# Performance work log

Hardware: AMD Instinct MI355X
Metric: run time of the kernel (lower is better)

Reference implementation:

```python
import jax, jax.numpy as jnp
import numpy as np

B, T, D, H, L, K = 64, 512, 256, 256, 2, 3


def setup_inputs() -> dict:
    key = jax.random.key(0)
    ks = jax.random.split(key, 12)
    s = 0.05
    f = jnp.float32
    return {
        "x": jax.random.normal(ks[0], (B, T, D), f),
        # GRUCell params per layer (torch gate order: r, z, n)
        "W_ih": jax.random.normal(ks[1], (L, 3 * H, H), f) * s,
        "b_ih": jax.random.normal(ks[2], (L, 3 * H), f) * s,
        "W_hh": jax.random.normal(ks[3], (L, 3 * H, H), f) * s,
        "b_hh": jax.random.normal(ks[4], (L, 3 * H), f) * s,
        # refinement cell params per layer
        "Wg": jax.random.normal(ks[5], (L, H, 2 * H), f) * s,
        "bg": jax.random.normal(ks[6], (L, H), f) * s,
        "Wt": jax.random.normal(ks[7], (L, H, 2 * H), f) * s,
        "bt": jax.random.normal(ks[8], (L, H), f) * s,
        "Wu": jax.random.normal(ks[9], (L, H, H), f) * s,
        "bu": jax.random.normal(ks[10], (L, H), f) * s,
    }


def reference(x, W_ih, b_ih, W_hh, b_hh, Wg, bg, Wt, bt, Wu, bu):
    def step(hidden, x_t):  # hidden: (L, B, H), x_t: (B, D)
        inp = x_t
        new_hiddens = []
        for l in range(L):
            h = hidden[l]
            # GRU cell (torch semantics)
            gi = inp @ W_ih[l].T + b_ih[l]
            gh = h @ W_hh[l].T + b_hh[l]
            i_r, i_z, i_n = jnp.split(gi, 3, axis=-1)
            h_r, h_z, h_n = jnp.split(gh, 3, axis=-1)
            r = jax.nn.sigmoid(i_r + h_r)
            z = jax.nn.sigmoid(i_z + h_z)
            n = jnp.tanh(i_n + r * h_n)
            h_new = (1.0 - z) * n + z * h
            # recursive refinement
            out = h_new
            rh = h_new
            for _ in range(K):
                comb = jnp.concatenate([out, rh], axis=-1)  # (B, 2H)
                g = jax.nn.sigmoid(comb @ Wg[l].T + bg[l])
                ref = jnp.tanh(comb @ Wt[l].T + bt[l])
                out = g * ref + (1.0 - g) * out
                rh = jnp.tanh(out @ Wu[l].T + bu[l])
            new_hiddens.append(h_new)
            inp = out
        return jnp.stack(new_hiddens, axis=0), inp

    hidden0 = jnp.zeros((L, B, H), x.dtype)
    final_hidden, outs = jax.lax.scan(step, hidden0, jnp.swapaxes(x, 0, 1))
    output = jnp.swapaxes(outs, 0, 1)  # (B, T, H)
    return output, final_hidden
```

## Files before the change

### kernel.cpp

```cpp
#include <hip/hip_runtime.h>

typedef float  f32x4  __attribute__((ext_vector_type(4)));
typedef __bf16 bf16x8 __attribute__((ext_vector_type(8)));

#define NB 64
#define NT 512
#define ND 256
#define NH 256
#define NROW (NB*NT)

#define OFF_WIH 0
#define OFF_WHH 393216
#define OFF_WGT 786432
#define OFF_WU  1310720
#define W_TOTAL 1441792
#define OFF_GI   (W_TOTAL)
#define OFF_OUT0 (OFF_GI + 512*64*768)
#define OFF_OUT1 (OFF_OUT0 + NROW*256)
#define OFF_FLAG (OFF_OUT1 + NROW*256)

#define NW 192

__device__ inline unsigned short f2bu(float f){
  unsigned int u = __builtin_bit_cast(unsigned int, f);
  unsigned int r = u + 0x7fffu + ((u >> 16) & 1u);
  return (unsigned short)(r >> 16);
}
__device__ inline float bf2f(unsigned short u){
  unsigned int v = ((unsigned int)u) << 16;
  return __builtin_bit_cast(float, v);
}
__device__ inline float sigm(float x){ return 1.0f / (1.0f + __expf(-x)); }
__device__ inline float tanhf_(float x){ return 1.0f - 2.0f / (__expf(2.0f * x) + 1.0f); }

#define MFMA(a,b,c) __builtin_amdgcn_mfma_f32_16x16x32_bf16((a),(b),(c),0,0,0)

__device__ inline void gload_lds16(const void* g, void* l){
  __builtin_amdgcn_global_load_lds(
    (const __attribute__((address_space(1))) unsigned int*)g,
    (__attribute__((address_space(3))) unsigned int*)l, 16, 0, 0);
}
__device__ inline bf16x8 ldG(const unsigned short* p){
  return *reinterpret_cast<const bf16x8*>(p);
}
template<int SLP>
__device__ inline void spin_ge(int* p, int tgt){
  while (__hip_atomic_load(p, __ATOMIC_RELAXED, __HIP_MEMORY_SCOPE_AGENT) < tgt)
    __builtin_amdgcn_s_sleep(SLP);
}

__global__ void cvt_weights(const float* __restrict__ Wih, const float* __restrict__ Whh,
                            const float* __restrict__ Wg,  const float* __restrict__ Wt,
                            const float* __restrict__ Wu,  unsigned short* __restrict__ ws){
  int i = blockIdx.x * blockDim.x + threadIdx.x;
  if (i < OFF_WHH) {
    ws[i] = f2bu(Wih[i]);
  } else if (i < OFF_WGT) {
    ws[i] = f2bu(Whh[i - OFF_WHH]);
  } else if (i < OFF_WU) {
    int j = i - OFF_WGT;
    int l = j >> 18; int r = (j >> 9) & 511; int k = j & 511;
    float v = (r < 256) ? Wg[(l * 256 + r) * 512 + k]
                        : Wt[(l * 256 + (r - 256)) * 512 + k];
    ws[i] = f2bu(v);
  } else if (i < W_TOTAL) {
    ws[i] = f2bu(Wu[i - OFF_WU]);
  }
}

__global__ void pack_x(const float* __restrict__ x, unsigned short* __restrict__ xin){
  size_t i = ((size_t)blockIdx.x * blockDim.x + threadIdx.x) * 4;
  float4 v = *reinterpret_cast<const float4*>(x + i);
  ushort4 u; u.x = f2bu(v.x); u.y = f2bu(v.y); u.z = f2bu(v.z); u.w = f2bu(v.w);
  *reinterpret_cast<ushort4*>(xin + i) = u;
}

__global__ __launch_bounds__(1024) void gi_gemm(
    const unsigned short* __restrict__ xin,
    const unsigned short* __restrict__ wih,
    const float* __restrict__ bih, const float* __restrict__ bhh,
    unsigned short* __restrict__ gi)
{
  __shared__ alignas(16) unsigned short sA[64 * 256];
  const int tid = threadIdx.x, blk = blockIdx.x;
  const int ln = tid & 63, wv = tid >> 6, m = ln & 15, lg = ln >> 4;
  {
    const char* src = (const char*)(xin + (size_t)blk * 64 * 256);
    #pragma unroll
    for (int i = 0; i < 2; ++i){
      int o = tid * 16 + i * 16384;
      int r = o >> 9, wb = o & 511;
      gload_lds16(src + (size_t)r * 512 + (wb ^ ((r & 7) << 4)), (char*)sA + o);
    }
  }
  __syncthreads();
  f32x4 acc[3][4] = {};
  #pragma unroll
  for (int kc = 0; kc < 8; ++kc){
    int kk = kc * 32 + lg * 8;
    bf16x8 a[4];
    #pragma unroll
    for (int mt = 0; mt < 4; ++mt){
      int row = mt * 16 + m;
      a[mt] = *(const bf16x8*)((const char*)sA + row * 512 + ((kk * 2) ^ ((row & 7) << 4)));
    }
    #pragma unroll
    for (int g = 0; g < 3; ++g){
      bf16x8 b = ldG(wih + (size_t)(g * 256 + wv * 16 + m) * 256 + kk);
      #pragma unroll
      for (int mt = 0; mt < 4; ++mt) acc[g][mt] = MFMA(a[mt], b, acc[g][mt]);
    }
  }
  const int c = wv * 16 + m;
  #pragma unroll
  for (int g = 0; g < 3; ++g){
    float bias = bih[g * 256 + c] + (g < 2 ? bhh[g * 256 + c] : 0.f);
    #pragma unroll
    for (int mt = 0; mt < 4; ++mt){
      #pragma unroll
      for (int j = 0; j < 4; ++j){
        int row = blk * 64 + mt * 16 + lg * 4 + j;
        int b = row >> 9, t = row & 511;
        gi[((size_t)t * 64 + b) * 768 + g * 256 + c] = f2bu(acc[g][mt][j] + bias);
      }
    }
  }
}

__device__ void chain_role(
    int grp, const unsigned short* __restrict__ gi, const unsigned short* __restrict__ whh,
    const float* __restrict__ bhh, unsigned short* __restrict__ outw,
    float* __restrict__ hfin, int* prog, int* bd, char* smem)
{
  __builtin_amdgcn_s_setprio(1);
  char* hAc = smem;
  const int tid = threadIdx.x;
  const int ln  = tid & 63, wv = tid >> 6;
  const int m   = ln & 15;
  const int lg  = ln >> 4;

  f32x4 wf[3][2][8];
  #pragma unroll
  for (int g = 0; g < 3; ++g)
    #pragma unroll
    for (int s = 0; s < 2; ++s){
      const unsigned short* p = whh + (size_t)(g * 256 + wv * 32 + s * 16 + m) * 256;
      #pragma unroll
      for (int kc = 0; kc < 8; ++kc){
        wf[g][s][kc] = *reinterpret_cast<const f32x4*>(p + kc * 32 + lg * 8);
        asm volatile("" : "+v"(wf[g][s][kc]));
      }
    }

  const int bb   = lg & 1;
  const int su   = lg >> 1;
  const int wcol = wv * 32 + su * 16 + m;
  const int brow = grp * 2 + bb;
  const float bNv = bhh[512 + wcol];

  const int arow  = m & 1;
  const int arows = arow << 4;
  const int rbase = arow * 512;
  const int wbyte = bb * 512 + ((wcol * 2) ^ (bb << 4));

  const unsigned short* gbase = gi + (size_t)brow * 768 + wcol;
  unsigned short* op = outw + (size_t)brow * NT * 256 + wcol;

  if (tid < 256){
    ((unsigned int*)hAc)[tid] = 0;
    ((unsigned int*)(hAc + 1024))[tid] = 0;
  }
  if (bd){
    if (tid == 0){ spin_ge<8>(&bd[0], 16); spin_ge<8>(&bd[1], 16); __threadfence(); }
    __syncthreads();
    (void)__hip_atomic_load(&bd[0], __ATOMIC_ACQUIRE, __HIP_MEMORY_SCOPE_AGENT);
  }
  unsigned int gAr = gbase[0], gAz = gbase[256], gAn = gbase[512];
  unsigned int gBr = gbase[49152], gBz = gbase[49152 + 256], gBn = gbase[49152 + 512];
  float h = 0.f;
  __syncthreads();

  auto body = [&](int t, int curo, unsigned int& GR, unsigned int& GZ, unsigned int& GN){
    float xr = bf2f((unsigned short)GR);
    float xz = bf2f((unsigned short)GZ);
    float xn = bf2f((unsigned short)GN);
    if (t + 2 < NT){
      const unsigned short* gp = gbase + (size_t)(t + 2) * 49152;
      GR = gp[0]; GZ = gp[256]; GN = gp[512];
    }
    f32x4 a00{}, a01{}, a10{}, a11{}, a20{}, a21{};
    #pragma unroll
    for (int kc = 0; kc < 8; ++kc){
      int kb = kc * 64 + lg * 16;
      bf16x8 hv = *(const bf16x8*)(hAc + curo + rbase + (kb ^ arows));
      a00 = MFMA(hv, __builtin_bit_cast(bf16x8, wf[0][0][kc]), a00);
      a01 = MFMA(hv, __builtin_bit_cast(bf16x8, wf[0][1][kc]), a01);
      a10 = MFMA(hv, __builtin_bit_cast(bf16x8, wf[1][0][kc]), a10);
      a11 = MFMA(hv, __builtin_bit_cast(bf16x8, wf[1][1][kc]), a11);
      a20 = MFMA(hv, __builtin_bit_cast(bf16x8, wf[2][0][kc]), a20);
      a21 = MFMA(hv, __builtin_bit_cast(bf16x8, wf[2][1][kc]), a21);
    }
    float aR = su ? (bb ? a01[1] : a01[0]) : (bb ? a00[1] : a00[0]);
    float aZ = su ? (bb ? a11[1] : a11[0]) : (bb ? a10[1] : a10[0]);
    float aN = su ? (bb ? a21[1] : a21[0]) : (bb ? a20[1] : a20[0]);
    float R = sigm(aR + xr);
    float Z = sigm(aZ + xz);
    float N = tanhf_(xn + R * (aN + bNv));
    h = N + Z * (h - N);
    unsigned short hb = f2bu(h);
    *(unsigned short*)(hAc + (curo ^ 1024) + wbyte) = hb;
    op[t * 256] = hb;
    asm volatile("s_waitcnt lgkmcnt(0)" ::: "memory");
    __builtin_amdgcn_sched_barrier(0);
    __builtin_amdgcn_s_barrier();
    __builtin_amdgcn_sched_barrier(0);
  };

  for (int tp = 0; tp < NT; tp += 2){
    if ((tp & 15) == 0){
      if (tp > 0){
        __syncthreads();
        if (tid == 0){
          __threadfence();
          __hip_atomic_store(prog, tp, __ATOMIC_RELEASE, __HIP_MEMORY_SCOPE_AGENT);
        }
      }
      if (bd){
        int B1 = (tp >> 4) + 1;
        if (B1 < 32){
          if (tid == 0){ spin_ge<8>(&bd[B1], 16); __threadfence(); }
          __syncthreads();
          (void)__hip_atomic_load(&bd[B1], __ATOMIC_ACQUIRE, __HIP_MEMORY_SCOPE_AGENT);
        }
      }
    }
    body(tp,     0,    gAr, gAz, gAn);
    body(tp + 1, 1024, gBr, gBz, gBn);
  }
  __syncthreads();
  if (tid == 0){
    __threadfence();
    __hip_atomic_store(prog, NT, __ATOMIC_RELEASE, __HIP_MEMORY_SCOPE_AGENT);
  }
  hfin[(size_t)brow * 256 + wcol] = h;
}

__device__ void worker_role(
    int w, unsigned short* __restrict__ gi,
    const unsigned short* __restrict__ outw0, const unsigned short* __restrict__ outw1,
    const unsigned short* __restrict__ wsb,
    const float* __restrict__ bih, const float* __restrict__ bhh,
    const float* __restrict__ bg, const float* __restrict__ bt, const float* __restrict__ bu,
    float* __restrict__ o, int* flags, char* smem)
{
  const int tid = threadIdx.x;
  const int ln = tid & 63, wv = tid >> 6, m = ln & 15, lg = ln >> 4;

  auto ldA = [&](int row, int kbyte) -> bf16x8 {
    return *(const bf16x8*)(smem + row * 1024 + (kbyte ^ ((row & 7) << 4)));
  };

  for (int i = w; i < 1024; i += NW){
    const int lay = i >> 9, t = i & 511;
    int* prog = &flags[lay * 32];
    if (tid == 0){
      for (int q = 0; q < 32; ++q) spin_ge<32>(&prog[q], t + 1);
      __threadfence();
    }
    __syncthreads();
    (void)__hip_atomic_load(&prog[0], __ATOMIC_ACQUIRE, __HIP_MEMORY_SCOPE_AGENT);

    const unsigned short* src0 = lay ? outw1 : outw0;
    #pragma unroll
    for (int q = 0; q < 8; ++q){
      int ofs = tid * 16 + q * 8192;
      int r = ofs >> 10, wb = ofs & 1023;
      int wb2 = (wb ^ ((r & 7) << 4)) & 511;
      gload_lds16((const char*)(src0 + ((size_t)r * NT + t) * 256) + wb2, smem + ofs);
    }
    __syncthreads();

    const unsigned short* wgt = wsb + OFF_WGT + (size_t)lay * 512 * 512;
    const unsigned short* wu  = wsb + OFF_WU  + (size_t)lay * 256 * 256;
    const float* bgp = bg + lay * 256;
    const float* btp = bt + lay * 256;
    const float* bup = bu + lay * 256;

    for (int iter = 0; iter < 3; ++iter){
      float oo0[4][4], oo1[4][4];
      {
        f32x4 ag[4] = {}, at4[4] = {};
        #pragma unroll 2
        for (int kc = 0; kc < 16; ++kc){
          int kk = kc * 32 + lg * 8;
          bf16x8 Bg = ldG(wgt + (size_t)(      wv * 32 + m) * 512 + kk);
          bf16x8 Bt = ldG(wgt + (size_t)(256 + wv * 32 + m) * 512 + kk);
          #pragma unroll
          for (int mt = 0; mt < 4; ++mt){
            bf16x8 A = ldA(mt * 16 + m, kk * 2);
            ag[mt]  = MFMA(A, Bg, ag[mt]);
            at4[mt] = MFMA(A, Bt, at4[mt]);
          }
        }
        int col = wv * 32 + m;
        float bgv = bgp[col], btv = btp[col];
        #pragma unroll
        for (int mt = 0; mt < 4; ++mt)
          #pragma unroll
          for (int j = 0; j < 4; ++j){
            int row = mt * 16 + lg * 4 + j;
            float old = bf2f(*(unsigned short*)(smem + row * 1024 + ((col * 2) ^ ((row & 7) << 4))));
            float g  = sigm(ag[mt][j] + bgv);
            float rf = tanhf_(at4[mt][j] + btv);
            oo0[mt][j] = g * rf + (1.f - g) * old;
          }
      }
      {
        f32x4 ag[4] = {}, at4[4] = {};
        #pragma unroll 2
        for (int kc = 0; kc < 16; ++kc){
          int kk = kc * 32 + lg * 8;
          bf16x8 Bg = ldG(wgt + (size_t)(      wv * 32 + 16 + m) * 512 + kk);
          bf16x8 Bt = ldG(wgt + (size_t)(256 + wv * 32 + 16 + m) * 512 + kk);
          #pragma unroll
          for (int mt = 0; mt < 4; ++mt){
            bf16x8 A = ldA(mt * 16 + m, kk * 2);
            ag[mt]  = MFMA(A, Bg, ag[mt]);
            at4[mt] = MFMA(A, Bt, at4[mt]);
          }
        }
        int col = wv * 32 + 16 + m;
        float bgv = bgp[col], btv = btp[col];
        #pragma unroll
        for (int mt = 0; mt < 4; ++mt)
          #pragma unroll
          for (int j = 0; j < 4; ++j){
            int row = mt * 16 + lg * 4 + j;
            float old = bf2f(*(unsigned short*)(smem + row * 1024 + ((col * 2) ^ ((row & 7) << 4))));
            float g  = sigm(ag[mt][j] + bgv);
            float rf = tanhf_(at4[mt][j] + btv);
            oo1[mt][j] = g * rf + (1.f - g) * old;
          }
      }
      __syncthreads();
      if (iter == 2 && lay == 1){
        #pragma unroll
        for (int mt = 0; mt < 4; ++mt)
          #pragma unroll
          for (int j = 0; j < 4; ++j){
            int b = mt * 16 + lg * 4 + j;
            o[((size_t)b * NT + t) * 256 + wv * 32 + m]      = oo0[mt][j];
            o[((size_t)b * NT + t) * 256 + wv * 32 + 16 + m] = oo1[mt][j];
          }
      } else {
        #pragma unroll
        for (int mt = 0; mt < 4; ++mt)
          #pragma unroll
          for (int j = 0; j < 4; ++j){
            int row = mt * 16 + lg * 4 + j;
            int c0 = wv * 32 + m, c1 = wv * 32 + 16 + m;
            *(unsigned short*)(smem + row * 1024 + ((c0 * 2) ^ ((row & 7) << 4))) = f2bu(oo0[mt][j]);
            *(unsigned short*)(smem + row * 1024 + ((c1 * 2) ^ ((row & 7) << 4))) = f2bu(oo1[mt][j]);
          }
        __syncthreads();
        if (iter < 2){
          #pragma unroll
          for (int s = 0; s < 2; ++s){
            f32x4 au[4] = {};
            #pragma unroll
            for (int kc = 0; kc < 8; ++kc){
              int kk = kc * 32 + lg * 8;
              bf16x8 Bu = ldG(wu + (size_t)(wv * 32 + s * 16 + m) * 256 + kk);
              #pragma unroll
              for (int mt = 0; mt < 4; ++mt)
                au[mt] = MFMA(ldA(mt * 16 + m, kk * 2), Bu, au[mt]);
            }
            int col = wv * 32 + s * 16 + m;
            float buv = bup[col];
            #pragma unroll
            for (int mt = 0; mt < 4; ++mt)
              #pragma unroll
              for (int j = 0; j < 4; ++j){
                int row = mt * 16 + lg * 4 + j;
                *(unsigned short*)(smem + row * 1024 + (((512 + col * 2)) ^ ((row & 7) << 4)))
                    = f2bu(tanhf_(au[mt][j] + buv));
              }
          }
          __syncthreads();
        }
      }
    }
    if (lay == 0){
      const unsigned short* wih1 = wsb + OFF_WIH + (size_t)768 * 256;
      #pragma unroll
      for (int q = 0; q < 6; ++q){
        int tile = wv + 8 * q;
        int cg = tile * 16 + m;
        f32x4 acc[4] = {};
        #pragma unroll
        for (int kc = 0; kc < 8; ++kc){
          int kk = kc * 32 + lg * 8;
          bf16x8 B = ldG(wih1 + (size_t)cg * 256 + kk);
          #pragma unroll
          for (int mt = 0; mt < 4; ++mt)
            acc[mt] = MFMA(ldA(mt * 16 + m, kk * 2), B, acc[mt]);
        }
        float bias = bih[768 + cg] + (cg < 512 ? bhh[768 + cg] : 0.f);
        #pragma unroll
        for (int mt = 0; mt < 4; ++mt)
          #pragma unroll
          for (int j = 0; j < 4; ++j){
            int b = mt * 16 + lg * 4 + j;
            gi[((size_t)t * 64 + b) * 768 + cg] = f2bu(acc[mt][j] + bias);
          }
      }
      __syncthreads();
      if (tid == 0){
        __threadfence();
        __hip_atomic_fetch_add(&flags[64 + (t >> 4)], 1, __ATOMIC_RELEASE, __HIP_MEMORY_SCOPE_AGENT);
      }
    } else {
      __syncthreads();
    }
  }
}

__global__ __launch_bounds__(512, 2) void mega(
    unsigned short* __restrict__ gi, const unsigned short* __restrict__ wsb,
    const float* __restrict__ bih, const float* __restrict__ bhh,
    const float* __restrict__ bg, const float* __restrict__ bt, const float* __restrict__ bu,
    unsigned short* __restrict__ outw0, unsigned short* __restrict__ outw1,
    float* __restrict__ o, float* __restrict__ hf, int* flags)
{
  __shared__ char smem[65536];
  const int role = blockIdx.x;
  if (role < NW){
    worker_role(role, gi, outw0, outw1, wsb, bih, bhh, bg, bt, bu, o, flags, smem);
  } else if (role < NW + 32){
    chain_role(role - NW, gi, wsb + OFF_WHH, bhh, outw0, hf,
               &flags[role - NW], nullptr, smem);
  } else {
    chain_role(role - NW - 32, gi, wsb + OFF_WHH + 768 * 256, bhh + 768, outw1,
               hf + 64 * 256, &flags[32 + (role - NW - 32)], &flags[64], smem);
  }
}

extern "C" void kernel_launch(void* const* d_in, const int* in_sizes, int n_in,
                              void* d_out, int out_size, void* d_ws, size_t ws_size,
                              hipStream_t stream) {
  const float* x   = (const float*)d_in[0];
  const float* Wih = (const float*)d_in[1];
  const float* bih = (const float*)d_in[2];
  const float* Whh = (const float*)d_in[3];
  const float* bhh = (const float*)d_in[4];
  const float* Wg  = (const float*)d_in[5];
  const float* bg  = (const float*)d_in[6];
  const float* Wt  = (const float*)d_in[7];
  const float* bt  = (const float*)d_in[8];
  const float* Wu  = (const float*)d_in[9];
  const float* bu  = (const float*)d_in[10];
  unsigned short* ws = (unsigned short*)d_ws;
  float* o  = (float*)d_out;
  float* hf = o + (size_t)NB * NT * NH;

  unsigned short* gi    = ws + OFF_GI;
  unsigned short* outw0 = ws + OFF_OUT0;
  unsigned short* outw1 = ws + OFF_OUT1;
  unsigned short* xin   = ws + OFF_OUT1;
  int* flags = (int*)(ws + OFF_FLAG);

  cvt_weights<<<W_TOTAL / 256, 256, 0, stream>>>(Wih, Whh, Wg, Wt, Wu, ws);
  pack_x<<<(NROW * 256 / 4) / 256, 256, 0, stream>>>(x, xin);
  gi_gemm<<<512, 1024, 0, stream>>>(xin, ws + OFF_WIH, bih, bhh, gi);
  (void)hipMemsetAsync(flags, 0, 96 * sizeof(int), stream);
  mega<<<256, 512, 0, stream>>>(gi, ws, bih, bhh, bg, bt, bu, outw0, outw1, o, hf, flags);
}
```

Before: 985.4 us.

## Pin refinement workers to chain groups with per-group 16-step flags

Workers no longer take whole timesteps for all 64 batch rows after waiting on every chain group. Each of 64 workers is now tied to one layer and one 2-row chain group, and processes 16-timestep blocks once that single group's progress flag is reached. Per-group handshake flags replace the shared counters, so layer-1 chains wait only on their own group's gi block. The grid drops to 128 blocks with chains placed first. Each MFMA tile now covers 32 rows instead of 64, and the worker count falls, so per-worker weight reuse drops and the refinement work per worker rises.

```diff
diff --git a/kernel.cpp b/kernel.cpp
--- a/kernel.cpp
+++ b/kernel.cpp
@@ -18,8 +18,6 @@
 #define OFF_OUT0 (OFF_GI + 512*64*768)
 #define OFF_OUT1 (OFF_OUT0 + NROW*256)
 #define OFF_FLAG (OFF_OUT1 + NROW*256)
-
-#define NW 192
 
 __device__ inline unsigned short f2bu(float f){
   unsigned int u = __builtin_bit_cast(unsigned int, f);
@@ -130,7 +128,7 @@
 __device__ void chain_role(
     int grp, const unsigned short* __restrict__ gi, const unsigned short* __restrict__ whh,
     const float* __restrict__ bhh, unsigned short* __restrict__ outw,
-    float* __restrict__ hfin, int* prog, int* bd, char* smem)
+    float* __restrict__ hfin, int* prog, int* fl, char* smem)
 {
   __builtin_amdgcn_s_setprio(1);
   char* hAc = smem;
@@ -170,10 +168,10 @@
     ((unsigned int*)hAc)[tid] = 0;
     ((unsigned int*)(hAc + 1024))[tid] = 0;
   }
-  if (bd){
-    if (tid == 0){ spin_ge<8>(&bd[0], 16); spin_ge<8>(&bd[1], 16); __threadfence(); }
+  if (fl){
+    if (tid == 0){ spin_ge<8>(&fl[0], 1); spin_ge<8>(&fl[1], 1); __threadfence(); }
     __syncthreads();
-    (void)__hip_atomic_load(&bd[0], __ATOMIC_ACQUIRE, __HIP_MEMORY_SCOPE_AGENT);
+    (void)__hip_atomic_load(&fl[0], __ATOMIC_ACQUIRE, __HIP_MEMORY_SCOPE_AGENT);
   }
   unsigned int gAr = gbase[0], gAz = gbase[256], gAn = gbase[512];
   unsigned int gBr = gbase[49152], gBz = gbase[49152 + 256], gBn = gbase[49152 + 512];
@@ -225,12 +223,12 @@
           __hip_atomic_store(prog, tp, __ATOMIC_RELEASE, __HIP_MEMORY_SCOPE_AGENT);
         }
       }
-      if (bd){
+      if (fl){
         int B1 = (tp >> 4) + 1;
         if (B1 < 32){
-          if (tid == 0){ spin_ge<8>(&bd[B1], 16); __threadfence(); }
+          if (tid == 0){ spin_ge<8>(&fl[B1], 1); __threadfence(); }
           __syncthreads();
-          (void)__hip_atomic_load(&bd[B1], __ATOMIC_ACQUIRE, __HIP_MEMORY_SCOPE_AGENT);
+          (void)__hip_atomic_load(&fl[B1], __ATOMIC_ACQUIRE, __HIP_MEMORY_SCOPE_AGENT);
         }
       }
     }
@@ -255,48 +253,48 @@
 {
   const int tid = threadIdx.x;
   const int ln = tid & 63, wv = tid >> 6, m = ln & 15, lg = ln >> 4;
+  const int q = w & 31, lay = w >> 5;
+  const int b0 = 2 * q;
+
+  int* prog = &flags[lay * 32 + q];
+  const unsigned short* src = lay ? outw1 : outw0;
+  const unsigned short* wgt = wsb + OFF_WGT + (size_t)lay * 512 * 512;
+  const unsigned short* wu  = wsb + OFF_WU  + (size_t)lay * 256 * 256;
+  const float* bgp = bg + lay * 256;
+  const float* btp = bt + lay * 256;
+  const float* bup = bu + lay * 256;
 
   auto ldA = [&](int row, int kbyte) -> bf16x8 {
     return *(const bf16x8*)(smem + row * 1024 + (kbyte ^ ((row & 7) << 4)));
   };
 
-  for (int i = w; i < 1024; i += NW){
-    const int lay = i >> 9, t = i & 511;
-    int* prog = &flags[lay * 32];
-    if (tid == 0){
-      for (int q = 0; q < 32; ++q) spin_ge<32>(&prog[q], t + 1);
-      __threadfence();
-    }
+  for (int B = 0; B < 32; ++B){
+    const int t0 = B * 16;
+    if (tid == 0){ spin_ge<32>(prog, t0 + 16); __threadfence(); }
     __syncthreads();
-    (void)__hip_atomic_load(&prog[0], __ATOMIC_ACQUIRE, __HIP_MEMORY_SCOPE_AGENT);
-
-    const unsigned short* src0 = lay ? outw1 : outw0;
-    #pragma unroll
-    for (int q = 0; q < 8; ++q){
-      int ofs = tid * 16 + q * 8192;
+    (void)__hip_atomic_load(prog, __ATOMIC_ACQUIRE, __HIP_MEMORY_SCOPE_AGENT);
+
+    #pragma unroll
+    for (int i = 0; i < 4; ++i){
+      int ofs = tid * 16 + i * 8192;
       int r = ofs >> 10, wb = ofs & 1023;
       int wb2 = (wb ^ ((r & 7) << 4)) & 511;
-      gload_lds16((const char*)(src0 + ((size_t)r * NT + t) * 256) + wb2, smem + ofs);
+      size_t grow = (size_t)(b0 + (r >> 4)) * NT + t0 + (r & 15);
+      gload_lds16((const char*)(src + grow * 256) + wb2, smem + ofs);
     }
     __syncthreads();
 
-    const unsigned short* wgt = wsb + OFF_WGT + (size_t)lay * 512 * 512;
-    const unsigned short* wu  = wsb + OFF_WU  + (size_t)lay * 256 * 256;
-    const float* bgp = bg + lay * 256;
-    const float* btp = bt + lay * 256;
-    const float* bup = bu + lay * 256;
-
     for (int iter = 0; iter < 3; ++iter){
-      float oo0[4][4], oo1[4][4];
+      float oo0[2][4], oo1[2][4];
       {
-        f32x4 ag[4] = {}, at4[4] = {};
+        f32x4 ag[2] = {}, at4[2] = {};
         #pragma unroll 2
         for (int kc = 0; kc < 16; ++kc){
           int kk = kc * 32 + lg * 8;
           bf16x8 Bg = ldG(wgt + (size_t)(      wv * 32 + m) * 512 + kk);
           bf16x8 Bt = ldG(wgt + (size_t)(256 + wv * 32 + m) * 512 + kk);
           #pragma unroll
-          for (int mt = 0; mt < 4; ++mt){
+          for (int mt = 0; mt < 2; ++mt){
             bf16x8 A = ldA(mt * 16 + m, kk * 2);
             ag[mt]  = MFMA(A, Bg, ag[mt]);
             at4[mt] = MFMA(A, Bt, at4[mt]);
@@ -305,7 +303,7 @@
         int col = wv * 32 + m;
         float bgv = bgp[col], btv = btp[col];
         #pragma unroll
-        for (int mt = 0; mt < 4; ++mt)
+        for (int mt = 0; mt < 2; ++mt)
           #pragma unroll
           for (int j = 0; j < 4; ++j){
             int row = mt * 16 + lg * 4 + j;
@@ -316,14 +314,14 @@
           }
       }
       {
-        f32x4 ag[4] = {}, at4[4] = {};
+        f32x4 ag[2] = {}, at4[2] = {};
         #pragma unroll 2
         for (int kc = 0; kc < 16; ++kc){
           int kk = kc * 32 + lg * 8;
           bf16x8 Bg = ldG(wgt + (size_t)(      wv * 32 + 16 + m) * 512 + kk);
           bf16x8 Bt = ldG(wgt + (size_t)(256 + wv * 32 + 16 + m) * 512 + kk);
           #pragma unroll
-          for (int mt = 0; mt < 4; ++mt){
+          for (int mt = 0; mt < 2; ++mt){
             bf16x8 A = ldA(mt * 16 + m, kk * 2);
             ag[mt]  = MFMA(A, Bg, ag[mt]);
             at4[mt] = MFMA(A, Bt, at4[mt]);
@@ -332,7 +330,7 @@
         int col = wv * 32 + 16 + m;
         float bgv = bgp[col], btv = btp[col];
         #pragma unroll
-        for (int mt = 0; mt < 4; ++mt)
+        for (int mt = 0; mt < 2; ++mt)
           #pragma unroll
           for (int j = 0; j < 4; ++j){
             int row = mt * 16 + lg * 4 + j;
@@ -345,16 +343,17 @@
       __syncthreads();
       if (iter == 2 && lay == 1){
         #pragma unroll
-        for (int mt = 0; mt < 4; ++mt)
+        for (int mt = 0; mt < 2; ++mt)
           #pragma unroll
           for (int j = 0; j < 4; ++j){
-            int b = mt * 16 + lg * 4 + j;
-            o[((size_t)b * NT + t) * 256 + wv * 32 + m]      = oo0[mt][j];
-            o[((size_t)b * NT + t) * 256 + wv * 32 + 16 + m] = oo1[mt][j];
+            int r = mt * 16 + lg * 4 + j;
+            size_t go = ((size_t)(b0 + mt) * NT + t0 + (r & 15)) * 256;
+            o[go + wv * 32 + m]      = oo0[mt][j];
+            o[go + wv * 32 + 16 + m] = oo1[mt][j];
           }
       } else {
         #pragma unroll
-        for (int mt = 0; mt < 4; ++mt)
+        for (int mt = 0; mt < 2; ++mt)
           #pragma unroll
           for (int j = 0; j < 4; ++j){
             int row = mt * 16 + lg * 4 + j;
@@ -366,19 +365,19 @@
         if (iter < 2){
           #pragma unroll
           for (int s = 0; s < 2; ++s){
-            f32x4 au[4] = {};
+            f32x4 au[2] = {};
             #pragma unroll
             for (int kc = 0; kc < 8; ++kc){
               int kk = kc * 32 + lg * 8;
               bf16x8 Bu = ldG(wu + (size_t)(wv * 32 + s * 16 + m) * 256 + kk);
               #pragma unroll
-              for (int mt = 0; mt < 4; ++mt)
+              for (int mt = 0; mt < 2; ++mt)
                 au[mt] = MFMA(ldA(mt * 16 + m, kk * 2), Bu, au[mt]);
             }
             int col = wv * 32 + s * 16 + m;
             float buv = bup[col];
             #pragma unroll
-            for (int mt = 0; mt < 4; ++mt)
+            for (int mt = 0; mt < 2; ++mt)
               #pragma unroll
               for (int j = 0; j < 4; ++j){
                 int row = mt * 16 + lg * 4 + j;
@@ -393,31 +392,29 @@
     if (lay == 0){
       const unsigned short* wih1 = wsb + OFF_WIH + (size_t)768 * 256;
       #pragma unroll
-      for (int q = 0; q < 6; ++q){
-        int tile = wv + 8 * q;
-        int cg = tile * 16 + m;
-        f32x4 acc[4] = {};
+      for (int qt = 0; qt < 6; ++qt){
+        int cg = (wv + 8 * qt) * 16 + m;
+        f32x4 acc[2] = {};
         #pragma unroll
         for (int kc = 0; kc < 8; ++kc){
           int kk = kc * 32 + lg * 8;
-          bf16x8 B = ldG(wih1 + (size_t)cg * 256 + kk);
-          #pragma unroll
-          for (int mt = 0; mt < 4; ++mt)
-            acc[mt] = MFMA(ldA(mt * 16 + m, kk * 2), B, acc[mt]);
+          bf16x8 Bf = ldG(wih1 + (size_t)cg * 256 + kk);
+          acc[0] = MFMA(ldA(m, kk * 2), Bf, acc[0]);
+          acc[1] = MFMA(ldA(16 + m, kk * 2), Bf, acc[1]);
         }
         float bias = bih[768 + cg] + (cg < 512 ? bhh[768 + cg] : 0.f);
         #pragma unroll
-        for (int mt = 0; mt < 4; ++mt)
+        for (int mt = 0; mt < 2; ++mt)
           #pragma unroll
           for (int j = 0; j < 4; ++j){
-            int b = mt * 16 + lg * 4 + j;
-            gi[((size_t)t * 64 + b) * 768 + cg] = f2bu(acc[mt][j] + bias);
+            int r = mt * 16 + lg * 4 + j;
+            gi[((size_t)(t0 + (r & 15)) * 64 + b0 + mt) * 768 + cg] = f2bu(acc[mt][j] + bias);
           }
       }
       __syncthreads();
       if (tid == 0){
         __threadfence();
-        __hip_atomic_fetch_add(&flags[64 + (t >> 4)], 1, __ATOMIC_RELEASE, __HIP_MEMORY_SCOPE_AGENT);
+        __hip_atomic_store(&flags[64 + q * 32 + B], 1, __ATOMIC_RELEASE, __HIP_MEMORY_SCOPE_AGENT);
       }
     } else {
       __syncthreads();
@@ -434,14 +431,14 @@
 {
   __shared__ char smem[65536];
   const int role = blockIdx.x;
-  if (role < NW){
-    worker_role(role, gi, outw0, outw1, wsb, bih, bhh, bg, bt, bu, o, flags, smem);
-  } else if (role < NW + 32){
-    chain_role(role - NW, gi, wsb + OFF_WHH, bhh, outw0, hf,
-               &flags[role - NW], nullptr, smem);
+  if (role < 32){
+    chain_role(role, gi, wsb + OFF_WHH, bhh, outw0, hf, &flags[role], nullptr, smem);
+  } else if (role < 64){
+    const int q = role - 32;
+    chain_role(q, gi, wsb + OFF_WHH + 768 * 256, bhh + 768, outw1,
+               hf + 64 * 256, &flags[32 + q], &flags[64 + q * 32], smem);
   } else {
-    chain_role(role - NW - 32, gi, wsb + OFF_WHH + 768 * 256, bhh + 768, outw1,
-               hf + 64 * 256, &flags[32 + (role - NW - 32)], &flags[64], smem);
+    worker_role(role - 64, gi, outw0, outw1, wsb, bih, bhh, bg, bt, bu, o, flags, smem);
   }
 }
 
@@ -472,6 +469,6 @@
   cvt_weights<<<W_TOTAL / 256, 256, 0, stream>>>(Wih, Whh, Wg, Wt, Wu, ws);
   pack_x<<<(NROW * 256 / 4) / 256, 256, 0, stream>>>(x, xin);
   gi_gemm<<<512, 1024, 0, stream>>>(xin, ws + OFF_WIH, bih, bhh, gi);
-  (void)hipMemsetAsync(flags, 0, 96 * sizeof(int), stream);
-  mega<<<256, 512, 0, stream>>>(gi, ws, bih, bhh, bg, bt, bu, outw0, outw1, o, hf, flags);
-}
+  (void)hipMemsetAsync(flags, 0, (64 + 1024) * sizeof(int), stream);
+  mega<<<128, 512, 0, stream>>>(gi, ws, bih, bhh, bg, bt, bu, outw0, outw1, o, hf, flags);
+}
```

After: 2.617 ms. 2.66x slower.
